# Performance work log

Hardware: AMD Instinct MI355X
Metric: run time of the kernel (lower is better)

The kernel has to match this reference:

```python
import jax, jax.numpy as jnp
import numpy as np

N_IN = 100000
N_OUT = 100000
NNZ = 3200000
B = 32
D = 32  # per-channel layer dim for Kaiming init


def setup_inputs() -> dict:
    key = jax.random.key(0)
    k1, k2, k3, k4 = jax.random.split(key, 4)
    x = jax.random.normal(k1, (B, N_IN, 1), dtype=jnp.float32)
    # COO indices: row 0 = src (into N_IN), row 1 = dst (into N_OUT)
    src = jax.random.randint(k2, (NNZ,), 0, N_IN, dtype=jnp.int64 if jax.config.jax_enable_x64 else jnp.int32)
    dst = jax.random.randint(k3, (NNZ,), 0, N_OUT, dtype=src.dtype)
    indices = jnp.stack([src, dst], axis=0)
    # Kaiming-style init: randn * sqrt(2/d)
    values = jax.random.normal(k4, (NNZ,), dtype=jnp.float32) * np.float32((2.0 / D) ** 0.5)
    bias = jnp.zeros((N_OUT, 1), dtype=jnp.float32)
    return {"x": x, "values": values, "bias": bias, "indices": indices, "n_out": N_OUT}


def reference(x, values, bias, indices, n_out):
    # (W^T @ x)[j] = sum_{e: dst[e]==j} values[e] * x[src[e]]
    src, dst = indices[0], indices[1]
    xg = x[:, :, 0][:, src]                 # (B, E) gather by src
    contrib = xg * values                   # (B, E)
    out = jax.ops.segment_sum(contrib.T, dst, num_segments=n_out)  # (N_out, B)
    return jnp.transpose(out)[:, :, None] + bias  # (B, N_out, 1) + (N_out,1) broadcast
```

## Files before the change

kernel.cpp:

```cpp
#include <hip/hip_runtime.h>


#define TJ 64
#define TJ_LOG 6
#define PACK_SHIFT 17
#define SRC_MASK ((1u << PACK_SHIFT) - 1u)
#define NSB_MAX 1600
#define CAP 8
#define A1_THREADS 512
#define A1_PER_THREAD 8
#define A1_BATCH (A1_THREADS * A1_PER_THREAD)
#define CHUNK 2048
#define GT 512
#define OVF_CAP 65536

__device__ __forceinline__ unsigned short f32_to_bf16_rn(float f) {
    unsigned u = __float_as_uint(f);
    unsigned r = (u + 0x7FFFu + ((u >> 16) & 1u)) >> 16;
    return (unsigned short)r;
}

__global__ void xpose_in_kernel(const float* __restrict__ x, unsigned short* __restrict__ xTh,
                                int N) {
    __shared__ float tile[32][33];
    int n0 = blockIdx.x * 32;
    int tx = threadIdx.x;
    int ty = threadIdx.y;
    if (n0 + tx < N) tile[ty][tx] = x[ty * (long)N + n0 + tx];
    __syncthreads();
    if (n0 + ty < N) xTh[(long)(n0 + ty) * 32 + tx] = f32_to_bf16_rn(tile[tx][ty]);
}

__global__ void init_cur_kernel(int* __restrict__ cur, int* __restrict__ ovf_cnt,
                                int nsb, int caps) {
    int i = blockIdx.x * blockDim.x + threadIdx.x;
    if (i < nsb) cur[i] = i * caps;
    if (i == 0) *ovf_cnt = 0;
}

__global__ __launch_bounds__(A1_THREADS) void partition_kernel(
        const int* __restrict__ src, const int* __restrict__ dst,
        const float* __restrict__ val, int* __restrict__ cur,
        uint2* __restrict__ binA, uint4* __restrict__ ovf, int* __restrict__ ovf_cnt,
        int nnz, int nsb, int caps) {
    __shared__ uint2 stage[NSB_MAX * CAP];
    __shared__ int scount[NSB_MAX];
    for (int i = threadIdx.x; i < nsb; i += A1_THREADS) scount[i] = 0;
    __syncthreads();

    for (long base = (long)blockIdx.x * A1_BATCH; base < nnz;
         base += (long)gridDim.x * A1_BATCH) {
        uint2 rec[A1_PER_THREAD];
        int bkt[A1_PER_THREAD];
        bool placed[A1_PER_THREAD];
        int rem = 0;
#pragma unroll
        for (int q = 0; q < A1_PER_THREAD; ++q) placed[q] = true;

        int e0 = (int)base + threadIdx.x * A1_PER_THREAD;
        if (e0 < nnz) {
            if (e0 + A1_PER_THREAD <= nnz) {
                const int4* s4 = (const int4*)(src + e0);
                const int4* d4 = (const int4*)(dst + e0);
                const float4* v4 = (const float4*)(val + e0);
                int4 sa = s4[0], sb = s4[1];
                int4 da = d4[0], db = d4[1];
                float4 va = v4[0], vb = v4[1];
                int ss[8] = {sa.x, sa.y, sa.z, sa.w, sb.x, sb.y, sb.z, sb.w};
                int dd[8] = {da.x, da.y, da.z, da.w, db.x, db.y, db.z, db.w};
                float vv[8] = {va.x, va.y, va.z, va.w, vb.x, vb.y, vb.z, vb.w};
#pragma unroll
                for (int q = 0; q < 8; ++q) {
                    rec[q] = make_uint2((unsigned)ss[q] | ((unsigned)(dd[q] & (TJ - 1)) << PACK_SHIFT),
                                        __float_as_uint(vv[q]));
                    bkt[q] = dd[q] >> TJ_LOG;
                    placed[q] = false;
                    ++rem;
                }
            } else {
#pragma unroll
                for (int q = 0; q < 8; ++q) {
                    int e = e0 + q;
                    if (e < nnz) {
                        int d = dst[e];
                        rec[q] = make_uint2((unsigned)src[e] | ((unsigned)(d & (TJ - 1)) << PACK_SHIFT),
                                            __float_as_uint(val[e]));
                        bkt[q] = d >> TJ_LOG;
                        placed[q] = false;
                        ++rem;
                    }
                }
            }
        }

        while (true) {
#pragma unroll
            for (int q = 0; q < A1_PER_THREAD; ++q) {
                if (!placed[q]) {
                    int slot = atomicAdd(&scount[bkt[q]], 1);
                    if (slot < CAP) {
                        stage[bkt[q] * CAP + slot] = rec[q];
                        placed[q] = true;
                        --rem;
                    }
                }
            }
            __syncthreads();
            for (int t = threadIdx.x; t < nsb; t += A1_THREADS) {
                int cc = scount[t];
                if (cc > CAP) cc = CAP;
                if (cc > 0) {
                    int g = atomicAdd(&cur[t], cc);
                    int cap_end = (t + 1) * caps;
                    int room = cap_end - g;
                    if (room < 0) room = 0;
                    int nfit = cc < room ? cc : room;
                    for (int q = 0; q < nfit; ++q) binA[g + q] = stage[t * CAP + q];
                    if (nfit < cc) {
                        int nsp = cc - nfit;
                        int ob = atomicAdd(ovf_cnt, nsp);
                        for (int q = nfit; q < cc; ++q, ++ob) {
                            if (ob < OVF_CAP) {
                                uint2 r = stage[t * CAP + q];
                                ovf[ob] = make_uint4(r.x & SRC_MASK,
                                                     (unsigned)(t * TJ) + (r.x >> PACK_SHIFT),
                                                     r.y, 0u);
                            }
                        }
                    }
                }
                scount[t] = 0;
            }
            if (__syncthreads_count(rem) == 0) break;
        }
    }
}

__global__ __launch_bounds__(GT) void gather_sort_kernel(
        const uint2* __restrict__ binA, const int* __restrict__ cur, int caps,
        const unsigned short* __restrict__ xTh, const float* __restrict__ bias,
        float* __restrict__ out, int n_out) {
    __shared__ __align__(16) char smem_raw[CHUNK * sizeof(uint2)];
    __shared__ __align__(16) char smem_srt[CHUNK * sizeof(uint2)];
    __shared__ int jhw[8 * TJ];
    __shared__ int joff[TJ], jend[TJ];
    uint2* raw = (uint2*)smem_raw;
    uint2* srt = (uint2*)smem_srt;
    float (*tile)[34] = (float (*)[34])smem_raw;

    int c = blockIdx.x;
    int j0 = c << TJ_LOG;
    int tid = threadIdx.x;
    int wv = tid >> 6, lane = tid & 63;
    int q = lane >> 4;
    int p = lane & 15;
    int k0 = wv * 8;

    float acc0[8], acc1[8];
#pragma unroll
    for (int k = 0; k < 8; ++k) { acc0[k] = 0.0f; acc1[k] = 0.0f; }

    int pos = c * caps;
    int end = cur[c];
    int cap_end = pos + caps;
    if (end > cap_end) end = cap_end;
    while (pos < end) {
        int n = min(CHUNK, end - pos);
        for (int i = tid; i < 8 * TJ; i += GT) jhw[i] = 0;
        __syncthreads();
        for (int i = tid; i < n; i += GT) {
            uint2 r = binA[pos + i];
            raw[i] = r;
            atomicAdd(&jhw[(wv << TJ_LOG) + (r.x >> PACK_SHIFT)], 1);
        }
        __syncthreads();
        if (tid < 64) {
            int basew[8];
            int tot = 0;
#pragma unroll
            for (int w = 0; w < 8; ++w) { basew[w] = tot; tot += jhw[(w << TJ_LOG) + tid]; }
            int inc = tot;
            for (int d = 1; d < 64; d <<= 1) {
                int t = __shfl_up(inc, d, 64);
                if (lane >= d) inc += t;
            }
            int off = inc - tot;
            joff[tid] = off;
            jend[tid] = off + tot;
#pragma unroll
            for (int w = 0; w < 8; ++w) jhw[(w << TJ_LOG) + tid] = off + basew[w];
        }
        __syncthreads();
        for (int i = tid; i < n; i += GT) {
            uint2 r = raw[i];
            int jl = (int)(r.x >> PACK_SHIFT);
            int pcur = atomicAdd(&jhw[(wv << TJ_LOG) + jl], 1);
            srt[pcur] = r;
        }
        __syncthreads();
#pragma unroll
        for (int k = 0; k < 8; ++k) {
            int kk = k0 + k;
            int t = joff[kk] + q;
            int t1 = jend[kk];
            float a0 = 0.0f, a1 = 0.0f;
            for (; t + 4 < t1; t += 8) {
                uint2 r0 = srt[t];
                uint2 r1 = srt[t + 4];
                unsigned u0 = *(const unsigned*)(xTh + (((int)(r0.x & SRC_MASK)) << 5) + (p << 1));
                unsigned u1 = *(const unsigned*)(xTh + (((int)(r1.x & SRC_MASK)) << 5) + (p << 1));
                float v0 = __uint_as_float(r0.y);
                float v1 = __uint_as_float(r1.y);
                a0 += v0 * __uint_as_float(u0 << 16);
                a1 += v0 * __uint_as_float(u0 & 0xFFFF0000u);
                a0 += v1 * __uint_as_float(u1 << 16);
                a1 += v1 * __uint_as_float(u1 & 0xFFFF0000u);
            }
            for (; t < t1; t += 4) {
                uint2 r = srt[t];
                unsigned u = *(const unsigned*)(xTh + (((int)(r.x & SRC_MASK)) << 5) + (p << 1));
                float v = __uint_as_float(r.y);
                a0 += v * __uint_as_float(u << 16);
                a1 += v * __uint_as_float(u & 0xFFFF0000u);
            }
            acc0[k] += a0;
            acc1[k] += a1;
        }
        __syncthreads();
        pos += n;
    }

#pragma unroll
    for (int k = 0; k < 8; ++k) {
        float a0 = acc0[k];
        a0 += __shfl_xor(a0, 16);
        a0 += __shfl_xor(a0, 32);
        float a1 = acc1[k];
        a1 += __shfl_xor(a1, 16);
        a1 += __shfl_xor(a1, 32);
        if (q == 0) {
            tile[k0 + k][(p << 1)]     = a0;
            tile[k0 + k][(p << 1) + 1] = a1;
        }
    }
    __syncthreads();
    for (int i = tid; i < TJ * 32; i += GT) {
        int bb = i >> TJ_LOG;
        int jl = i & (TJ - 1);
        int j = j0 + jl;
        if (j < n_out) out[bb * n_out + j] = tile[jl][bb] + bias[j];
    }
}

__global__ void fixup_kernel(const uint4* __restrict__ ovf, const int* __restrict__ ovf_cnt,
                             const unsigned short* __restrict__ xTh,
                             float* __restrict__ out, int n_out) {
    int cnt = *ovf_cnt;
    if (cnt > OVF_CAP) cnt = OVF_CAP;
    int total = cnt * 32;
    int tid = blockIdx.x * blockDim.x + threadIdx.x;
    int nth = gridDim.x * blockDim.x;
    for (int i = tid; i < total; i += nth) {
        uint4 r = ovf[i >> 5];
        int b = i & 31;
        float xv = __uint_as_float((unsigned)xTh[(r.x << 5) + b] << 16);
        atomicAdd(&out[(long)b * n_out + (int)r.y], __uint_as_float(r.z) * xv);
    }
}

__global__ void xpose_in_f32_kernel(const float* __restrict__ x, float* __restrict__ xT, int N) {
    __shared__ float tile[32][33];
    int n0 = blockIdx.x * 32;
    int tx = threadIdx.x;
    int ty = threadIdx.y;
    if (n0 + tx < N) tile[ty][tx] = x[ty * (long)N + n0 + tx];
    __syncthreads();
    if (n0 + ty < N) xT[(long)(n0 + ty) * 32 + tx] = tile[tx][ty];
}

__global__ void edge_kernel(const float* __restrict__ xT, const float* __restrict__ values,
                            const int* __restrict__ src, const int* __restrict__ dst,
                            float* __restrict__ accT, int nnz) {
    int tid = blockIdx.x * blockDim.x + threadIdx.x;
    int lane_b = tid & 31;
    int e0 = tid >> 5;
    int estride = (gridDim.x * blockDim.x) >> 5;
    for (int e = e0; e < nnz; e += estride) {
        atomicAdd(&accT[(long)dst[e] * 32 + lane_b], values[e] * xT[(long)src[e] * 32 + lane_b]);
    }
}

__global__ void xpose_out_kernel(const float* __restrict__ accT, const float* __restrict__ bias,
                                 float* __restrict__ out, int N) {
    __shared__ float tile[32][33];
    int j0 = blockIdx.x * 32;
    int tx = threadIdx.x;
    int ty = threadIdx.y;
    if (j0 + ty < N) tile[ty][tx] = accT[(long)(j0 + ty) * 32 + tx];
    __syncthreads();
    if (j0 + tx < N) out[ty * (long)N + j0 + tx] = tile[tx][ty] + bias[j0 + tx];
}

__global__ void edge_direct_kernel(const float* __restrict__ x, const float* __restrict__ values,
                                   const int* __restrict__ src, const int* __restrict__ dst,
                                   float* __restrict__ out, int nnz, int N_IN, int N_OUT) {
    int tid = blockIdx.x * blockDim.x + threadIdx.x;
    int lane_b = tid & 31;
    int e0 = tid >> 5;
    int estride = (gridDim.x * blockDim.x) >> 5;
    for (int e = e0; e < nnz; e += estride) {
        atomicAdd(&out[(long)lane_b * N_OUT + dst[e]],
                  values[e] * x[(long)lane_b * N_IN + src[e]]);
    }
}

__global__ void init_out_bias_kernel(float* __restrict__ out, const float* __restrict__ bias,
                                     int N_OUT, int B) {
    long i = (long)blockIdx.x * blockDim.x + threadIdx.x;
    if (i < (long)N_OUT * B) out[i] = bias[i % N_OUT];
}

extern "C" void kernel_launch(void* const* d_in, const int* in_sizes, int n_in,
                              void* d_out, int out_size, void* d_ws, size_t ws_size,
                              hipStream_t stream) {
    const float* x      = (const float*)d_in[0];
    const float* values = (const float*)d_in[1];
    const float* bias   = (const float*)d_in[2];
    const int*   idx    = (const int*)d_in[3];

    const int NNZ   = in_sizes[1];
    const int N_OUT = in_sizes[2];
    const int B     = out_size / N_OUT;
    const int N_IN  = in_sizes[0] / B;

    const int* src = idx;
    const int* dst = idx + NNZ;
    float* out = (float*)d_out;

    const int nsb = (N_OUT + TJ - 1) >> TJ_LOG;

    int caps = (NNZ + nsb - 1) / nsb + 384;
    caps = (caps + 7) & ~7;

    const size_t xTh_b  = (((size_t)N_IN * 32 * sizeof(unsigned short)) + 15) & ~(size_t)15;
    const size_t bin_b  = (size_t)nsb * caps * sizeof(uint2);
    const size_t cur_b  = (((size_t)nsb * sizeof(int)) + 15) & ~(size_t)15;
    const size_t ovf_b  = (size_t)OVF_CAP * sizeof(uint4);
    const size_t need   = xTh_b + bin_b + cur_b + ovf_b + 16;

    const bool shape_ok = (B == 32) && (NNZ > 0) && (nsb <= NSB_MAX) &&
                          (N_IN <= (1 << PACK_SHIFT));

    if (shape_ok && ws_size >= need) {
        char* p = (char*)d_ws;
        unsigned short* xTh = (unsigned short*)p;  p += xTh_b;
        uint2* binA = (uint2*)p;                   p += bin_b;
        int* cur = (int*)p;                        p += cur_b;
        uint4* ovf = (uint4*)p;                    p += ovf_b;
        int* ovf_cnt = (int*)p;

        {
            dim3 blk(32, 32);
            xpose_in_kernel<<<(N_IN + 31) / 32, blk, 0, stream>>>(x, xTh, N_IN);
        }
        init_cur_kernel<<<(nsb + 255) / 256, 256, 0, stream>>>(cur, ovf_cnt, nsb, caps);
        partition_kernel<<<256, A1_THREADS, 0, stream>>>(src, dst, values, cur, binA,
                                                         ovf, ovf_cnt, NNZ, nsb, caps);
        gather_sort_kernel<<<nsb, GT, 0, stream>>>(binA, cur, caps, xTh, bias, out, N_OUT);
        fixup_kernel<<<64, 256, 0, stream>>>(ovf, ovf_cnt, xTh, out, N_OUT);
    } else if (B == 32 && ws_size >= (size_t)N_IN * 32 * sizeof(float) +
                                     (size_t)N_OUT * 32 * sizeof(float)) {
        float* xT = (float*)d_ws;
        float* accT = (float*)((char*)d_ws + (size_t)N_IN * 32 * sizeof(float));
        dim3 blk(32, 32);
        xpose_in_f32_kernel<<<(N_IN + 31) / 32, blk, 0, stream>>>(x, xT, N_IN);
        hipMemsetAsync(accT, 0, (size_t)N_OUT * 32 * sizeof(float), stream);
        edge_kernel<<<4096, 256, 0, stream>>>(xT, values, src, dst, accT, NNZ);
        xpose_out_kernel<<<(N_OUT + 31) / 32, blk, 0, stream>>>(accT, bias, out, N_OUT);
    } else {
        long total = (long)N_OUT * B;
        init_out_bias_kernel<<<(int)((total + 255) / 256), 256, 0, stream>>>(out, bias, N_OUT, B);
        edge_direct_kernel<<<4096, 256, 0, stream>>>(x, values, src, dst, out, NNZ, N_IN, N_OUT);
    }
}
```

Measured before the change: 135.7 us.

## Drop LDS staging in partition; scatter records directly using per-bucket base offsets

The partition kernel no longer copies records into a large shared staging array and then out to global memory from one thread per bucket. Each thread instead keeps its slot index, the block reserves a global base per bucket with one atomic, and threads write their own records straight to the bin array. This frees about 100KB of LDS, so CAP can rise and the kernel can launch up to 1024 blocks with higher occupancy. The cost is scattered, uncoalesced 8-byte global writes in place of per-bucket contiguous runs, plus an extra barrier per round.

```diff
diff --git a/kernel.cpp b/kernel.cpp
--- a/kernel.cpp
+++ b/kernel.cpp
@@ -6,7 +6,7 @@
 #define PACK_SHIFT 17
 #define SRC_MASK ((1u << PACK_SHIFT) - 1u)
 #define NSB_MAX 1600
-#define CAP 8
+#define CAP 32
 #define A1_THREADS 512
 #define A1_PER_THREAD 8
 #define A1_BATCH (A1_THREADS * A1_PER_THREAD)
@@ -43,8 +43,8 @@
         const float* __restrict__ val, int* __restrict__ cur,
         uint2* __restrict__ binA, uint4* __restrict__ ovf, int* __restrict__ ovf_cnt,
         int nnz, int nsb, int caps) {
-    __shared__ uint2 stage[NSB_MAX * CAP];
     __shared__ int scount[NSB_MAX];
+    __shared__ int sbase[NSB_MAX];
     for (int i = threadIdx.x; i < nsb; i += A1_THREADS) scount[i] = 0;
     __syncthreads();
 
@@ -52,10 +52,9 @@
          base += (long)gridDim.x * A1_BATCH) {
         uint2 rec[A1_PER_THREAD];
         int bkt[A1_PER_THREAD];
-        bool placed[A1_PER_THREAD];
-        int rem = 0;
-#pragma unroll
-        for (int q = 0; q < A1_PER_THREAD; ++q) placed[q] = true;
+        int st[A1_PER_THREAD];
+#pragma unroll
+        for (int q = 0; q < A1_PER_THREAD; ++q) st[q] = -2;
 
         int e0 = (int)base + threadIdx.x * A1_PER_THREAD;
         if (e0 < nnz) {
@@ -74,8 +73,7 @@
                     rec[q] = make_uint2((unsigned)ss[q] | ((unsigned)(dd[q] & (TJ - 1)) << PACK_SHIFT),
                                         __float_as_uint(vv[q]));
                     bkt[q] = dd[q] >> TJ_LOG;
-                    placed[q] = false;
-                    ++rem;
+                    st[q] = -1;
                 }
             } else {
 #pragma unroll
@@ -86,8 +84,7 @@
                         rec[q] = make_uint2((unsigned)src[e] | ((unsigned)(d & (TJ - 1)) << PACK_SHIFT),
                                             __float_as_uint(val[e]));
                         bkt[q] = d >> TJ_LOG;
-                        placed[q] = false;
-                        ++rem;
+                        st[q] = -1;
                     }
                 }
             }
@@ -96,40 +93,40 @@
         while (true) {
 #pragma unroll
             for (int q = 0; q < A1_PER_THREAD; ++q) {
-                if (!placed[q]) {
-                    int slot = atomicAdd(&scount[bkt[q]], 1);
-                    if (slot < CAP) {
-                        stage[bkt[q] * CAP + slot] = rec[q];
-                        placed[q] = true;
-                        --rem;
-                    }
+                if (st[q] == -1) {
+                    int s = atomicAdd(&scount[bkt[q]], 1);
+                    if (s < CAP) st[q] = s;
                 }
             }
             __syncthreads();
             for (int t = threadIdx.x; t < nsb; t += A1_THREADS) {
                 int cc = scount[t];
-                if (cc > CAP) cc = CAP;
                 if (cc > 0) {
-                    int g = atomicAdd(&cur[t], cc);
-                    int cap_end = (t + 1) * caps;
-                    int room = cap_end - g;
-                    if (room < 0) room = 0;
-                    int nfit = cc < room ? cc : room;
-                    for (int q = 0; q < nfit; ++q) binA[g + q] = stage[t * CAP + q];
-                    if (nfit < cc) {
-                        int nsp = cc - nfit;
-                        int ob = atomicAdd(ovf_cnt, nsp);
-                        for (int q = nfit; q < cc; ++q, ++ob) {
-                            if (ob < OVF_CAP) {
-                                uint2 r = stage[t * CAP + q];
-                                ovf[ob] = make_uint4(r.x & SRC_MASK,
-                                                     (unsigned)(t * TJ) + (r.x >> PACK_SHIFT),
-                                                     r.y, 0u);
-                            }
+                    if (cc > CAP) cc = CAP;
+                    sbase[t] = atomicAdd(&cur[t], cc);
+                    scount[t] = 0;
+                }
+            }
+            __syncthreads();
+            int rem = 0;
+#pragma unroll
+            for (int q = 0; q < A1_PER_THREAD; ++q) {
+                if (st[q] >= 0) {
+                    int g = sbase[bkt[q]] + st[q];
+                    if (g < (bkt[q] + 1) * caps) {
+                        binA[g] = rec[q];
+                    } else {
+                        int ob = atomicAdd(ovf_cnt, 1);
+                        if (ob < OVF_CAP) {
+                            ovf[ob] = make_uint4(rec[q].x & SRC_MASK,
+                                                 (unsigned)(bkt[q] * TJ) + (rec[q].x >> PACK_SHIFT),
+                                                 rec[q].y, 0u);
                         }
                     }
-                }
-                scount[t] = 0;
+                    st[q] = -2;
+                } else if (st[q] == -1) {
+                    ++rem;
+                }
             }
             if (__syncthreads_count(rem) == 0) break;
         }
@@ -364,8 +361,13 @@
             xpose_in_kernel<<<(N_IN + 31) / 32, blk, 0, stream>>>(x, xTh, N_IN);
         }
         init_cur_kernel<<<(nsb + 255) / 256, 256, 0, stream>>>(cur, ovf_cnt, nsb, caps);
-        partition_kernel<<<256, A1_THREADS, 0, stream>>>(src, dst, values, cur, binA,
-                                                         ovf, ovf_cnt, NNZ, nsb, caps);
+        {
+            int nblk = (NNZ + A1_BATCH - 1) / A1_BATCH;
+            if (nblk > 1024) nblk = 1024;
+            if (nblk < 1) nblk = 1;
+            partition_kernel<<<nblk, A1_THREADS, 0, stream>>>(src, dst, values, cur, binA,
+                                                              ovf, ovf_cnt, NNZ, nsb, caps);
+        }
         gather_sort_kernel<<<nsb, GT, 0, stream>>>(binA, cur, caps, xTh, bias, out, N_OUT);
         fixup_kernel<<<64, 256, 0, stream>>>(ovf, ovf_cnt, xTh, out, N_OUT);
     } else if (B == 32 && ws_size >= (size_t)N_IN * 32 * sizeof(float) +
```

After: 136.0 us. About the same (+0.2%).
